# Kernel tuning notes

Measured on AMD Instinct MI355X. Metric: run time of the kernel, lower is better.

Reference implementation:

```python
import jax, jax.numpy as jnp
import numpy as np

N_FEATURES = 1024
N_TOKENS = 65536


def _circulant(w):
    """C[i, j] = w[(j - i) mod n], matching torch circulant(tensor, 0).
    Example: w=[0,1,2] -> [[0,1,2],[2,0,1],[1,2,0]]."""
    n = w.shape[0]
    j = jnp.arange(n)[None, :]
    i = jnp.arange(n)[:, None]
    return w[(j - i) % n]  # [n, n]


def setup_inputs() -> dict:
    key = jax.random.key(0)
    kx, kw = jax.random.split(key)
    x = jax.random.normal(kx, (N_TOKENS, N_FEATURES), dtype=jnp.float32)
    # torch.rand -> uniform [0, 1)
    weight = jax.random.uniform(kw, (N_FEATURES,), dtype=jnp.float32)
    return {"x": x, "weight": weight}


def reference(x, weight):
    C = _circulant(weight)  # [n, n]
    # F.linear(x, C) = x @ C.T  ->  mm[b, i] = sum_j x[b, j] * C[i, j]
    mm_cx = jnp.einsum("bj,ij->bi", x, C)
    out = mm_cx * x + mm_cx + x
    return out
```

## Files before the change

kernel.cpp:

```cpp
#include <hip/hip_runtime.h>

typedef __attribute__((ext_vector_type(8))) _Float16 half8;
typedef __attribute__((ext_vector_type(4))) float f32x4;

#define NF       1024
#define BM       64
#define NTHREADS 1024
#define NSLABS   8
#define SLABK    128
#define WCOPY0   2048
#define WCOPYS   2040
#define WTOT     (WCOPY0 + 7 * WCOPYS)

__global__ __launch_bounds__(NTHREADS, 4)
void circ_kernel(const float* __restrict__ x, const float* __restrict__ wsrc,
                 float* __restrict__ out) {
    __shared__ __align__(16) _Float16 lds_A[128 * 64 * 8];
    __shared__ __align__(16) _Float16 lds_W[WTOT];

    const int tid  = threadIdx.x;
    const int bm   = blockIdx.x;
    const int lane = tid & 63;
    const int wv   = tid >> 6;
    const int l15  = lane & 15;
    const int quad = lane >> 4;

    for (int idx = tid; idx < WTOT; idx += NTHREADS) {
        int s, t;
        if (idx < WCOPY0) { s = 0; t = idx; }
        else { int r = idx - WCOPY0; s = 1 + r / WCOPYS; t = r - (s - 1) * WCOPYS; }
        lds_W[idx] = (_Float16)wsrc[(t + s) & (NF - 1)];
    }

    const int sr  = tid >> 4;
    const int skc = tid & 15;
    const float* xrow = x + ((size_t)(bm * BM + sr) << 10) + skc * 8;

    f32x4 st0 = *(const f32x4*)(xrow);
    f32x4 st1 = *(const f32x4*)(xrow + 4);

    auto write_slab = [&](int slab) {
        half8 h;
        #pragma unroll
        for (int e = 0; e < 4; ++e) h[e]     = (_Float16)st0[e];
        #pragma unroll
        for (int e = 0; e < 4; ++e) h[4 + e] = (_Float16)st1[e];
        int w = slab * 16 + skc;
        *(half8*)&lds_A[(w * 64 + sr) * 8] = h;
    };
    write_slab(0);

    int bbase0;
    {
        int icol = wv * 64 + l15;
        int o0   = 1024 + 8 * quad - icol;
        int s    = o0 & 7;
        int t0   = o0 - s;
        int offs = (s == 0) ? 0 : (WCOPY0 + (s - 1) * WCOPYS);
        bbase0 = offs + t0;
    }

    f32x4 acc[4][4];
    #pragma unroll
    for (int a = 0; a < 4; ++a)
        #pragma unroll
        for (int b = 0; b < 4; ++b)
            acc[a][b] = (f32x4){0.f, 0.f, 0.f, 0.f};

    __syncthreads();

    half8 bfr[4];
    #pragma unroll
    for (int f = 0; f < 4; ++f)
        bfr[f] = *(const half8*)&lds_W[bbase0 - 16 * f];

    for (int slab = 0; slab < NSLABS; ++slab) {
        if (slab + 1 < NSLABS) {
            const float* xs = xrow + (slab + 1) * SLABK;
            st0 = *(const f32x4*)(xs);
            st1 = *(const f32x4*)(xs + 4);
        }
        #pragma unroll
        for (int ks = 0; ks < 4; ++ks) {
            const int k0 = slab * SLABK + ks * 32;
            half8 afr[4];
            #pragma unroll
            for (int mf = 0; mf < 4; ++mf)
                afr[mf] = *(const half8*)&lds_A[(((k0 >> 3) + quad) * 64 + mf * 16 + l15) * 8];
            constexpr int ford[4] = {2, 3, 0, 1};
            #pragma unroll
            for (int mf = 0; mf < 4; ++mf)
                #pragma unroll
                for (int ff = 0; ff < 4; ++ff) {
                    const int f = ford[ff];
                    acc[mf][f] = __builtin_amdgcn_mfma_f32_16x16x32_f16(
                        afr[mf], bfr[(f - 2 * ks) & 3], acc[mf][f], 0, 0, 0);
                }
            if (ks < 3) {
                const int k0n = k0 + 32;
                bfr[(0 - 2 * (ks + 1)) & 3] = *(const half8*)&lds_W[bbase0 + k0n];
                bfr[(1 - 2 * (ks + 1)) & 3] = *(const half8*)&lds_W[bbase0 - 16 + k0n];
            }
        }
        if (slab + 1 < NSLABS) {
            const int k0n = (slab + 1) * SLABK;
            bfr[0] = *(const half8*)&lds_W[bbase0 + k0n];
            bfr[1] = *(const half8*)&lds_W[bbase0 - 16 + k0n];
            write_slab(slab + 1);
        }
        __syncthreads();
    }

    #pragma unroll
    for (int mf = 0; mf < 4; ++mf) {
        #pragma unroll
        for (int f = 0; f < 4; ++f) {
            int icol = wv * 64 + f * 16 + l15;
            f32x4 v = acc[mf][f];
            #pragma unroll
            for (int reg = 0; reg < 4; ++reg) {
                int m = mf * 16 + quad * 4 + reg;
                float xf = (float)lds_A[((icol >> 3) * 64 + m) * 8 + (icol & 7)];
                float mm = v[reg];
                out[((size_t)(bm * BM + m) << 10) + icol] = mm * xf + mm + xf;
            }
        }
    }
}

extern "C" void kernel_launch(void* const* d_in, const int* in_sizes, int n_in,
                              void* d_out, int out_size, void* d_ws, size_t ws_size,
                              hipStream_t stream) {
    const float* x = (const float*)d_in[0];
    const float* w = (const float*)d_in[1];
    float* o       = (float*)d_out;
    circ_kernel<<<dim3(65536 / BM), dim3(NTHREADS), 0, stream>>>(x, w, o);
}
```

Measured before the change: 470.4 us.

## Swap MFMA operand roles so epilogue writes contiguous float4 rows

The MFMA operands are swapped so the circulant weights become the A operand and the x tile the B operand. The accumulator layout then has consecutive output features per lane, which allows 16-byte vector stores of the output and half4 reads of x in the epilogue instead of scalar accesses. The x tile is stored row-major in LDS with an XOR swizzle to avoid bank conflicts, and the redundant final barrier is dropped. The swizzled addressing adds some index arithmetic, and bank behaviour of the new LDS read pattern may differ.

```diff
diff --git a/kernel.cpp b/kernel.cpp
--- a/kernel.cpp
+++ b/kernel.cpp
@@ -1,6 +1,7 @@
 #include <hip/hip_runtime.h>
 
 typedef __attribute__((ext_vector_type(8))) _Float16 half8;
+typedef __attribute__((ext_vector_type(4))) _Float16 half4;
 typedef __attribute__((ext_vector_type(4))) float f32x4;
 
 #define NF       1024
@@ -15,7 +16,7 @@
 __global__ __launch_bounds__(NTHREADS, 4)
 void circ_kernel(const float* __restrict__ x, const float* __restrict__ wsrc,
                  float* __restrict__ out) {
-    __shared__ __align__(16) _Float16 lds_A[128 * 64 * 8];
+    __shared__ __align__(16) _Float16 lds_X[64 * 1024];
     __shared__ __align__(16) _Float16 lds_W[WTOT];
 
     const int tid  = threadIdx.x;
@@ -24,6 +25,7 @@
     const int wv   = tid >> 6;
     const int l15  = lane & 15;
     const int quad = lane >> 4;
+    const int xk   = l15 & 7;
 
     for (int idx = tid; idx < WTOT; idx += NTHREADS) {
         int s, t;
@@ -46,18 +48,19 @@
         #pragma unroll
         for (int e = 0; e < 4; ++e) h[4 + e] = (_Float16)st1[e];
         int w = slab * 16 + skc;
-        *(half8*)&lds_A[(w * 64 + sr) * 8] = h;
+        int p = w ^ (sr & 7);
+        *(half8*)&lds_X[sr * 1024 + p * 8] = h;
     };
     write_slab(0);
 
-    int bbase0;
+    int abase0;
     {
-        int icol = wv * 64 + l15;
-        int o0   = 1024 + 8 * quad - icol;
+        int irow = wv * 64 + l15;
+        int o0   = 1024 + 8 * quad - irow;
         int s    = o0 & 7;
         int t0   = o0 - s;
         int offs = (s == 0) ? 0 : (WCOPY0 + (s - 1) * WCOPYS);
-        bbase0 = offs + t0;
+        abase0 = offs + t0;
     }
 
     f32x4 acc[4][4];
@@ -69,10 +72,10 @@
 
     __syncthreads();
 
-    half8 bfr[4];
+    half8 afr[4];
     #pragma unroll
-    for (int f = 0; f < 4; ++f)
-        bfr[f] = *(const half8*)&lds_W[bbase0 - 16 * f];
+    for (int m = 0; m < 4; ++m)
+        afr[m] = *(const half8*)&lds_W[abase0 - 16 * m];
 
     for (int slab = 0; slab < NSLABS; ++slab) {
         if (slab + 1 < NSLABS) {
@@ -83,47 +86,54 @@
         #pragma unroll
         for (int ks = 0; ks < 4; ++ks) {
             const int k0 = slab * SLABK + ks * 32;
-            half8 afr[4];
+            const int cb = slab * 16 + ks * 4;
+            half8 bx[4];
             #pragma unroll
-            for (int mf = 0; mf < 4; ++mf)
-                afr[mf] = *(const half8*)&lds_A[(((k0 >> 3) + quad) * 64 + mf * 16 + l15) * 8];
-            constexpr int ford[4] = {2, 3, 0, 1};
+            for (int f = 0; f < 4; ++f)
+                bx[f] = *(const half8*)
+                    &lds_X[(f * 16 + l15) * 1024 + (((cb + quad) ^ xk)) * 8];
+            constexpr int mord[4] = {2, 3, 0, 1};
             #pragma unroll
-            for (int mf = 0; mf < 4; ++mf)
+            for (int mm_ = 0; mm_ < 4; ++mm_) {
+                const int mf = mord[mm_];
                 #pragma unroll
-                for (int ff = 0; ff < 4; ++ff) {
-                    const int f = ford[ff];
+                for (int f = 0; f < 4; ++f)
                     acc[mf][f] = __builtin_amdgcn_mfma_f32_16x16x32_f16(
-                        afr[mf], bfr[(f - 2 * ks) & 3], acc[mf][f], 0, 0, 0);
-                }
+                        afr[(mf - 2 * ks) & 3], bx[f], acc[mf][f], 0, 0, 0);
+            }
             if (ks < 3) {
                 const int k0n = k0 + 32;
-                bfr[(0 - 2 * (ks + 1)) & 3] = *(const half8*)&lds_W[bbase0 + k0n];
-                bfr[(1 - 2 * (ks + 1)) & 3] = *(const half8*)&lds_W[bbase0 - 16 + k0n];
+                afr[(0 - 2 * (ks + 1)) & 3] = *(const half8*)&lds_W[abase0 + k0n];
+                afr[(1 - 2 * (ks + 1)) & 3] = *(const half8*)&lds_W[abase0 - 16 + k0n];
             }
         }
         if (slab + 1 < NSLABS) {
             const int k0n = (slab + 1) * SLABK;
-            bfr[0] = *(const half8*)&lds_W[bbase0 + k0n];
-            bfr[1] = *(const half8*)&lds_W[bbase0 - 16 + k0n];
+            afr[0] = *(const half8*)&lds_W[abase0 + k0n];
+            afr[1] = *(const half8*)&lds_W[abase0 - 16 + k0n];
             write_slab(slab + 1);
+            __syncthreads();
         }
-        __syncthreads();
     }
 
     #pragma unroll
     for (int mf = 0; mf < 4; ++mf) {
+        const int ib = wv * 64 + mf * 16 + quad * 4;
+        const int pc = (ib >> 3) ^ xk;
+        const int eo = ib & 7;
         #pragma unroll
         for (int f = 0; f < 4; ++f) {
-            int icol = wv * 64 + f * 16 + l15;
-            f32x4 v = acc[mf][f];
+            const int tok = f * 16 + l15;
+            half4 xv = *(const half4*)&lds_X[tok * 1024 + pc * 8 + eo];
+            f32x4 mmv = acc[mf][f];
+            f32x4 o;
             #pragma unroll
             for (int reg = 0; reg < 4; ++reg) {
-                int m = mf * 16 + quad * 4 + reg;
-                float xf = (float)lds_A[((icol >> 3) * 64 + m) * 8 + (icol & 7)];
-                float mm = v[reg];
-                out[((size_t)(bm * BM + m) << 10) + icol] = mm * xf + mm + xf;
+                float xf = (float)xv[reg];
+                float mm = mmv[reg];
+                o[reg] = mm * xf + mm + xf;
             }
+            *(f32x4*)&out[((size_t)(bm * BM + tok) << 10) + ib] = o;
         }
     }
 }
```

After: 485.4 us. 1.03x slower.
